# Kernel tuning notes

Hardware: AMD Instinct MI355X
Metric: run time of the kernel (lower is better)

## Reference

```python
import jax, jax.numpy as jnp
import numpy as np

N = 32768      # total nodes
E = 524288     # edges (avg degree 16)
HID = 256      # hidden_dim
H = 8          # heads
C = HID // H   # head dim = 32
G = 64         # graphs in batch
NPG = N // G   # nodes per graph = 512
EDIM = 2       # edge feature dim
NEG_SLOPE = 0.2  # PyG GATv2 default


def setup_inputs():
    key = jax.random.key(0)
    ks = jax.random.split(key, 12)
    s = 0.05
    return dict(
        x=jax.random.normal(ks[0], (N, HID), jnp.float32),
        edge_attr=jax.random.normal(ks[1], (E, EDIM), jnp.float32),
        # GATv2Conv params
        W_l=jax.random.normal(ks[2], (HID, HID), jnp.float32) * s,
        b_l=jnp.zeros((HID,), jnp.float32),
        W_r=jax.random.normal(ks[3], (HID, HID), jnp.float32) * s,
        b_r=jnp.zeros((HID,), jnp.float32),
        W_e=jax.random.normal(ks[4], (EDIM, HID), jnp.float32) * s,
        att=jax.random.normal(ks[5], (H, C), jnp.float32) * s,
        bias_gat=jnp.zeros((HID,), jnp.float32),
        # MultiheadAttention params (torch packed qkv layout)
        in_proj_w=jax.random.normal(ks[6], (3 * HID, HID), jnp.float32) * s,
        in_proj_b=jnp.zeros((3 * HID,), jnp.float32),
        out_proj_w=jax.random.normal(ks[7], (HID, HID), jnp.float32) * s,
        out_proj_b=jnp.zeros((HID,), jnp.float32),
        alpha_param=jnp.array(0.5, jnp.float32),
        # FFN
        W1=jax.random.normal(ks[8], (HID, 4 * HID), jnp.float32) * s,
        b1=jnp.zeros((4 * HID,), jnp.float32),
        W2=jax.random.normal(ks[9], (4 * HID, HID), jnp.float32) * s,
        b2=jnp.zeros((HID,), jnp.float32),
        # LayerNorms
        g1=jnp.ones((HID,), jnp.float32), be1=jnp.zeros((HID,), jnp.float32),
        g2=jnp.ones((HID,), jnp.float32), be2=jnp.zeros((HID,), jnp.float32),
        g3=jnp.ones((HID,), jnp.float32), be3=jnp.zeros((HID,), jnp.float32),
        edge_index=jax.random.randint(ks[10], (2, E), 0, N, jnp.int32),
        batch=jnp.repeat(jnp.arange(G, dtype=jnp.int32), NPG),
    )


def _ln(x, g, b, eps=1e-5):
    m = jnp.mean(x, -1, keepdims=True)
    v = jnp.mean((x - m) ** 2, -1, keepdims=True)
    return (x - m) * jax.lax.rsqrt(v + eps) * g + b


def _gatv2(x, edge_index, edge_attr, W_l, b_l, W_r, b_r, W_e, att, bias_gat):
    src, dst = edge_index[0], edge_index[1]
    # PyG add_self_loops with fill_value='mean': self-loop edge_attr at node i
    # is the mean of edge_attr over edges incoming to i (0 if none).
    deg = jax.ops.segment_sum(jnp.ones((E,), x.dtype), dst, num_segments=N)
    ea_mean = jax.ops.segment_sum(edge_attr, dst, num_segments=N) / jnp.maximum(deg, 1.0)[:, None]
    loop = jnp.arange(N, dtype=src.dtype)
    src2 = jnp.concatenate([src, loop])
    dst2 = jnp.concatenate([dst, loop])
    ea2 = jnp.concatenate([edge_attr, ea_mean], axis=0)  # [E+N, 2]
    xl = (x @ W_l + b_l).reshape(N, H, C)  # source transform (messages)
    xr = (x @ W_r + b_r).reshape(N, H, C)  # target transform
    ee = (ea2 @ W_e).reshape(-1, H, C)
    e = jax.nn.leaky_relu(xl[src2] + xr[dst2] + ee, NEG_SLOPE)  # [E+N, H, C]
    score = jnp.einsum('ehc,hc->eh', e, att)  # [E+N, H]
    # scatter softmax over incoming edges of each target node
    smax = jax.lax.stop_gradient(jax.ops.segment_max(score, dst2, num_segments=N))
    ex = jnp.exp(score - smax[dst2])
    ssum = jax.ops.segment_sum(ex, dst2, num_segments=N)
    alpha = ex / ssum[dst2]  # [E+N, H]
    out = jax.ops.segment_sum(alpha[:, :, None] * xl[src2], dst2, num_segments=N)
    return out.reshape(N, HID) + bias_gat


def _mha(xg, in_proj_w, in_proj_b, out_proj_w, out_proj_b):
    # xg: [G, NPG, HID]; torch nn.MultiheadAttention (batch_first, eval mode)
    qkv = xg @ in_proj_w.T + in_proj_b
    q, k, v = jnp.split(qkv, 3, axis=-1)
    q = q.reshape(G, NPG, H, C)
    k = k.reshape(G, NPG, H, C)
    v = v.reshape(G, NPG, H, C)
    scores = jnp.einsum('gqhd,gkhd->ghqk', q, k) / jnp.sqrt(jnp.float32(C))
    p = jax.nn.softmax(scores, axis=-1)
    o = jnp.einsum('ghqk,gkhd->gqhd', p, v).reshape(G, NPG, HID)
    return o @ out_proj_w.T + out_proj_b


def reference(x, edge_attr, W_l, b_l, W_r, b_r, W_e, att, bias_gat,
              in_proj_w, in_proj_b, out_proj_w, out_proj_b, alpha_param,
              W1, b1, W2, b2, g1, be1, g2, be2, g3, be3, edge_index, batch):
    local_out = _ln(
        _gatv2(x, edge_index, edge_attr, W_l, b_l, W_r, b_r, W_e, att, bias_gat),
        g1, be1)
    # batch is sorted with equal-sized graphs -> the per-graph ragged
    # attention loop equals one batched [G, NPG, NPG] attention
    xg = x.reshape(G, NPG, HID)
    global_out = _mha(xg, in_proj_w, in_proj_b, out_proj_w, out_proj_b).reshape(N, HID)
    global_out = _ln(global_out, g2, be2)
    a = jax.nn.sigmoid(alpha_param)
    combined = a * local_out + (1.0 - a) * global_out
    ffn = jax.nn.gelu(combined @ W1 + b1, approximate=False) @ W2 + b2
    return _ln(combined + ffn, g3, be3)
```

## Files before the change

kernel.cpp:

```cpp
#include <hip/hip_runtime.h>
#include <math.h>

#define N_NODES 32768
#define E_EDGES 524288
#define HIDDEN  256
#define NPG     512
#define NGRAPH  64
#define NHEAD   8
#define CDIM    32

typedef unsigned short bf16;
typedef __attribute__((ext_vector_type(8))) short short8;
typedef __attribute__((ext_vector_type(4))) float f4;

#define AS1 __attribute__((address_space(1)))
#define AS3 __attribute__((address_space(3)))

__device__ __forceinline__ void cp16(const bf16* g, bf16* l) {
    __builtin_amdgcn_global_load_lds((AS1 const unsigned int*)(const void*)g,
                                     (AS3 unsigned int*)(void*)l, 16, 0, 0);
}

__device__ inline float bf2f(unsigned short u) {
    union { unsigned int i; float f; } v; v.i = ((unsigned int)u) << 16; return v.f;
}
__device__ inline unsigned short f2bf(float f) {
    union { float f; unsigned int i; } v; v.f = f;
    unsigned int x = v.i;
    return (unsigned short)((x + 0x7FFFu + ((x >> 16) & 1u)) >> 16);
}
__device__ inline unsigned short f2bf_trunc(float f) {
    return (unsigned short)(__float_as_uint(f) >> 16);
}
__device__ inline float4 load4(const float* p) { return *(const float4*)p; }
__device__ inline float4 load4(const bf16* p) {
    ushort4 u = *(const ushort4*)p;
    return make_float4(bf2f(u.x), bf2f(u.y), bf2f(u.z), bf2f(u.w));
}
__device__ inline void store4(float* p, float4 v) { *(float4*)p = v; }
__device__ inline void store4(bf16* p, float4 v) {
    ushort4 u; u.x = f2bf(v.x); u.y = f2bf(v.y); u.z = f2bf(v.z); u.w = f2bf(v.w);
    *(ushort4*)p = u;
}


__global__ void zero_kernel(float* deg, float* ea_sum, int* fill) {
    int i = blockIdx.x * blockDim.x + threadIdx.x;
    if (i < 2 * N_NODES) ea_sum[i] = 0.0f;
    if (i < N_NODES) { deg[i] = 0.0f; fill[i] = 0; }
}

__global__ void deg_kernel(const int* __restrict__ ei, const float* __restrict__ edge_attr,
                           float* deg, float* ea_sum) {
    int e = blockIdx.x * blockDim.x + threadIdx.x;
    if (e >= E_EDGES) return;
    int d = ei[E_EDGES + e];
    atomicAdd(&deg[d], 1.0f);
    atomicAdd(&ea_sum[2 * d + 0], edge_attr[2 * e + 0]);
    atomicAdd(&ea_sum[2 * d + 1], edge_attr[2 * e + 1]);
}

__global__ __launch_bounds__(1024) void scan_kernel(const float* __restrict__ deg, int* row_ptr) {
    __shared__ int part[1024];
    int t = threadIdx.x;
    int base = t * 32;
    int loc[32];
    int s = 0;
    #pragma unroll
    for (int j = 0; j < 32; j++) {
        loc[j] = s;
        s += (int)deg[base + j] + 1;
    }
    int mysum = s;
    part[t] = s;
    __syncthreads();
    for (int off = 1; off < 1024; off <<= 1) {
        int v = 0;
        if (t >= off) v = part[t - off];
        __syncthreads();
        part[t] += v;
        __syncthreads();
    }
    int offset = part[t] - mysum;
    #pragma unroll
    for (int j = 0; j < 32; j++) row_ptr[base + j] = offset + loc[j];
    if (t == 1023) row_ptr[N_NODES] = part[1023];
}

__global__ void fill_kernel(const int* __restrict__ ei, const float* __restrict__ edge_attr,
                            const float* __restrict__ ea_sum, const float* __restrict__ deg,
                            const int* __restrict__ row_ptr, int* fill, int4* __restrict__ erec) {
    int tid = blockIdx.x * blockDim.x + threadIdx.x;
    if (tid >= E_EDGES + N_NODES) return;
    int d, src; float a0, a1;
    if (tid < E_EDGES) {
        d = ei[E_EDGES + tid];
        src = ei[tid];
        a0 = edge_attr[2 * tid + 0];
        a1 = edge_attr[2 * tid + 1];
    } else {
        d = tid - E_EDGES;
        src = d;
        float dm = fmaxf(deg[d], 1.0f);
        a0 = ea_sum[2 * d + 0] / dm;
        a1 = ea_sum[2 * d + 1] / dm;
    }
    int pos = row_ptr[d] + atomicAdd(&fill[d], 1);
    int4 r;
    r.x = src;
    r.y = __float_as_int(a0);
    r.z = __float_as_int(a1);
    r.w = 0;
    erec[pos] = r;
}

#define QSCALE 0.25506882685716462f
__global__ void convall(const float* __restrict__ x,
                        const float* __restrict__ W_l, const float* __restrict__ W_r,
                        const float* __restrict__ W1, const float* __restrict__ W2,
                        const float* __restrict__ in_proj_w, const float* __restrict__ out_proj_w,
                        const float* __restrict__ b_l, const float* __restrict__ b_r,
                        const float* __restrict__ in_proj_b,
                        bf16* xb, bf16* wcat, bf16* w1b, bf16* w2b,
                        bf16* wopb, float* bcat)
{
    int b = blockIdx.x, t = threadIdx.x;
    if (b < 8192) {
        int i = b * 256 + t;
        store4(&xb[i * 4], *(const float4*)&x[i * 4]);
    } else if (b < 8960) {
        int i = (b - 8192) * 256 + t;
        float v = in_proj_w[i];
        if (i < 65536) v *= QSCALE;
        wcat[i] = f2bf(v);
    } else if (b < 9216) {
        int i = (b - 8960) * 256 + t; int k = i >> 8, n = i & 255;
        wcat[(768 + n) * 256 + k] = f2bf(W_l[i]);
    } else if (b < 9472) {
        int i = (b - 9216) * 256 + t; int k = i >> 8, n = i & 255;
        wcat[(1024 + n) * 256 + k] = f2bf(W_r[i]);
    } else if (b < 10496) {
        int i = (b - 9472) * 256 + t; int k = i >> 10, n = i & 1023;
        w1b[n * 256 + k] = f2bf(W1[i]);
    } else if (b < 11520) {
        int i = (b - 10496) * 256 + t; int k = i >> 8, n = i & 255;
        w2b[n * 1024 + k] = f2bf(W2[i]);
    } else if (b < 11584) {
        int i = (b - 11520) * 256 + t;
        store4(&wopb[i * 4], *(const float4*)&out_proj_w[i * 4]);
    } else {
        #pragma unroll
        for (int j = 0; j < 5; j++) {
            int idx = j * 256 + t;
            float v;
            if (idx < 768) { v = in_proj_b[idx]; if (idx < 256) v *= QSCALE; }
            else if (idx < 1024) v = b_l[idx - 768];
            else v = b_r[idx - 1024];
            bcat[idx] = v;
        }
    }
}

template <int EPI>
__global__ __launch_bounds__(256) void mfma_gemm(
    const bf16* __restrict__ A, const bf16* __restrict__ Wb,
    const float* __restrict__ bias, const bf16* __restrict__ res,
    bf16* __restrict__ C, int M, int N, int K, bf16* __restrict__ d2)
{
    __shared__ bf16 lds[2 * 128 * 64];
    bf16* As = lds;
    bf16* Bs = lds + 128 * 64;
    int tid = threadIdx.x;
    int wave = tid >> 6, lane = tid & 63;
    int quad = lane >> 4, l16 = lane & 15;
    int n0 = blockIdx.x * 128, m0 = blockIdx.y * 128;
    int wm = (wave & 1) * 64, wn = (wave >> 1) * 64;

    f4 acc[4][4] = {};
    int srow = tid >> 3;
    int scol = (tid & 7) * 8;

    for (int k0 = 0; k0 < K; k0 += 64) {
        #pragma unroll
        for (int i = 0; i < 4; i++) {
            int row = i * 32 + srow;
            cp16(&A[(size_t)(m0 + row) * K + k0 + scol], &As[row * 64 + scol]);
            cp16(&Wb[(size_t)(n0 + row) * K + k0 + scol], &Bs[row * 64 + scol]);
        }
        __syncthreads();
        #pragma unroll
        for (int ks = 0; ks < 2; ks++) {
            short8 af[4], bfr[4];
            #pragma unroll
            for (int mt = 0; mt < 4; mt++)
                af[mt] = *(const short8*)&As[(wm + mt * 16 + l16) * 64 + ks * 32 + quad * 8];
            #pragma unroll
            for (int nt = 0; nt < 4; nt++)
                bfr[nt] = *(const short8*)&Bs[(wn + nt * 16 + l16) * 64 + ks * 32 + quad * 8];
            #pragma unroll
            for (int mt = 0; mt < 4; mt++)
                #pragma unroll
                for (int nt = 0; nt < 4; nt++)
                    acc[mt][nt] = __builtin_amdgcn_mfma_f32_16x16x32_bf16(
                        af[mt], bfr[nt], acc[mt][nt], 0, 0, 0);
        }
        __syncthreads();
    }

    float* epi = (float*)lds + wave * 16 * 68;
    int row = lane >> 2;
    int cb = (lane & 3) * 16;
    int gn = n0 + wn + cb;
    float bb[16];
    *(float4*)&bb[0]  = *(const float4*)&bias[gn + 0];
    *(float4*)&bb[4]  = *(const float4*)&bias[gn + 4];
    *(float4*)&bb[8]  = *(const float4*)&bias[gn + 8];
    *(float4*)&bb[12] = *(const float4*)&bias[gn + 12];

    for (int mt = 0; mt < 4; mt++) {
        #pragma unroll
        for (int nt = 0; nt < 4; nt++)
            #pragma unroll
            for (int r = 0; r < 4; r++)
                epi[(quad * 4 + r) * 68 + nt * 16 + l16] = acc[mt][nt][r];
        float vv[16];
        *(float4*)&vv[0]  = *(float4*)&epi[row * 68 + cb + 0];
        *(float4*)&vv[4]  = *(float4*)&epi[row * 68 + cb + 4];
        *(float4*)&vv[8]  = *(float4*)&epi[row * 68 + cb + 8];
        *(float4*)&vv[12] = *(float4*)&epi[row * 68 + cb + 12];
        int gm = m0 + wm + mt * 16 + row;
        #pragma unroll
        for (int j = 0; j < 16; j++) vv[j] += bb[j];
        if (EPI == 1) {
            #pragma unroll
            for (int j = 0; j < 16; j++)
                vv[j] = 0.5f * vv[j] * (1.0f + erff(vv[j] * 0.70710678118654752f));
        } else if (EPI == 4) {
            ushort rr[16];
            const bf16* rp = &res[(size_t)gm * N + gn];
            *(int4*)&rr[0] = *(const int4*)&rp[0];
            *(int4*)&rr[8] = *(const int4*)&rp[8];
            #pragma unroll
            for (int j = 0; j < 16; j++) vv[j] += bf2f(rr[j]);
            float* cf = (float*)C + (size_t)gm * N + gn;
            *(float4*)&cf[0]  = *(float4*)&vv[0];
            *(float4*)&cf[4]  = *(float4*)&vv[4];
            *(float4*)&cf[8]  = *(float4*)&vv[8];
            *(float4*)&cf[12] = *(float4*)&vv[12];
            continue;
        }
        ushort o16[16];
        #pragma unroll
        for (int j = 0; j < 16; j++) o16[j] = f2bf(vv[j]);
        bf16* cp;
        if (EPI == 5) {
            if (gn < 768) {
                cp = &C[(size_t)gm * 768 + gn];
            } else if (gn < 1024) {
                cp = &((bf16*)res)[(size_t)gm * 256 + (gn - 768)];
            } else {
                cp = &d2[(size_t)gm * 256 + (gn - 1024)];
            }
        } else {
            cp = &C[(size_t)gm * N + gn];
        }
        *(int4*)&cp[0] = *(int4*)&o16[0];
        *(int4*)&cp[8] = *(int4*)&o16[8];
    }
}

__global__ __launch_bounds__(256) void attn_mfma(
    const bf16* __restrict__ qkv, bf16* __restrict__ attnout)
{
    __shared__ bf16 Ks[128 * 40];
    __shared__ bf16 Vt[32 * 136];
    __shared__ bf16 Pb[4 * 64 * 40];

    int b = blockIdx.x;
    int g = b >> 4, h = (b >> 1) & 7, hlf = b & 1;
    int tid = threadIdx.x;
    int wave = tid >> 6, lane = tid & 63;
    int quad = lane >> 4, l16 = lane & 15;
    int qbase = hlf * 256 + wave * 64;
    bf16* Pw = &Pb[wave * 64 * 40];

    short8 qf[4];
    #pragma unroll
    for (int mt = 0; mt < 4; mt++) {
        size_t node = (size_t)(g * NPG + qbase + mt * 16 + l16);
        qf[mt] = *(const short8*)&qkv[node * 768 + h * CDIM + quad * 8];
    }

    f4 oacc[4][2] = {};
    float lacc[4][4] = {};

    for (int c = 0; c < 4; c++) {
        int kk0 = c * 128;
        __syncthreads();
        #pragma unroll
        for (int i = 0; i < 2; i++) {
            int idx = i * 256 + tid;
            int key = idx >> 2, kc = (idx & 3) * 8;
            *(int4*)&Ks[key * 40 + kc] =
                *(const int4*)&qkv[(size_t)(g * NPG + kk0 + key) * 768 + 256 + h * CDIM + kc];
        }
        {
            int key = tid >> 1, dblk = (tid & 1) * 16;
            ushort tmp[16];
            const bf16* vp = &qkv[(size_t)(g * NPG + kk0 + key) * 768 + 512 + h * CDIM + dblk];
            *(int4*)&tmp[0] = *(const int4*)&vp[0];
            *(int4*)&tmp[8] = *(const int4*)&vp[8];
            #pragma unroll
            for (int j = 0; j < 16; j++) Vt[(dblk + j) * 136 + key] = tmp[j];
        }
        __syncthreads();

        for (int sub = 0; sub < 4; sub++) {
            int ks0 = sub * 32;
            short8 kf[2];
            #pragma unroll
            for (int nt = 0; nt < 2; nt++)
                kf[nt] = *(const short8*)&Ks[(ks0 + nt * 16 + l16) * 40 + quad * 8];
            #pragma unroll
            for (int mt = 0; mt < 4; mt++) {
                #pragma unroll
                for (int nt = 0; nt < 2; nt++) {
                    f4 z = {0.f, 0.f, 0.f, 0.f};
                    f4 s = __builtin_amdgcn_mfma_f32_16x16x32_bf16(qf[mt], kf[nt], z, 0, 0, 0);
                    #pragma unroll
                    for (int r = 0; r < 4; r++) {
                        float p = exp2f(s[r]);
                        lacc[mt][r] += p;
                        Pw[(mt * 16 + quad * 4 + r) * 40 + nt * 16 + l16] = f2bf_trunc(p);
                    }
                }
            }
            short8 vf[2];
            #pragma unroll
            for (int dt = 0; dt < 2; dt++)
                vf[dt] = *(const short8*)&Vt[(dt * 16 + l16) * 136 + ks0 + quad * 8];
            #pragma unroll
            for (int mt = 0; mt < 4; mt++) {
                short8 pf = *(const short8*)&Pw[(mt * 16 + l16) * 40 + quad * 8];
                #pragma unroll
                for (int dt = 0; dt < 2; dt++)
                    oacc[mt][dt] = __builtin_amdgcn_mfma_f32_16x16x32_bf16(
                        pf, vf[dt], oacc[mt][dt], 0, 0, 0);
            }
        }
    }

    #pragma unroll
    for (int mt = 0; mt < 4; mt++)
        #pragma unroll
        for (int r = 0; r < 4; r++) {
            float l = lacc[mt][r];
            l += __shfl_xor(l, 1);
            l += __shfl_xor(l, 2);
            l += __shfl_xor(l, 4);
            l += __shfl_xor(l, 8);
            lacc[mt][r] = l;
        }

    #pragma unroll
    for (int mt = 0; mt < 4; mt++) {
        #pragma unroll
        for (int dt = 0; dt < 2; dt++) {
            #pragma unroll
            for (int r = 0; r < 4; r++) {
                float v = oacc[mt][dt][r] / lacc[mt][r];
                size_t node = (size_t)(g * NPG + qbase + mt * 16 + quad * 4 + r);
                attnout[node * HIDDEN + h * CDIM + dt * 16 + l16] = f2bf(v);
            }
        }
    }
}

__device__ __forceinline__ void fetchrec(
    int i, int re, int node, const int4* __restrict__ erec,
    int& s, float& a0, float& a1)
{
    if (i < re) {
        int4 r = erec[i];
        s = r.x; a0 = __int_as_float(r.y); a1 = __int_as_float(r.z);
    } else {
        s = node; a0 = 0.f; a1 = 0.f;
    }
}

__global__ __launch_bounds__(256) void gat_kernel(
    const bf16* __restrict__ xl, const bf16* __restrict__ xr,
    const int* __restrict__ row_ptr, const int4* __restrict__ erec,
    const float* __restrict__ W_e, const float* __restrict__ att,
    const float* __restrict__ bias_gat,
    const float* __restrict__ g1, const float* __restrict__ be1,
    bf16* __restrict__ out)
{
    __shared__ float pacc[2][260];
    __shared__ float plsum[2][64];
    int wave = threadIdx.x >> 6;
    int lane = threadIdx.x & 63;
    int nloc = wave >> 1, half = wave & 1;
    int node = blockIdx.x * 2 + nloc;
    int cb = lane * 4;

    float4 xr4 = load4(&xr[(size_t)node * 256 + cb]);
    float4 we0 = *(const float4*)&W_e[cb];
    float4 we1 = *(const float4*)&W_e[HIDDEN + cb];
    float4 at4 = *(const float4*)&att[cb];

    int rs = row_ptr[node], re = row_ptr[node + 1];

    float lsum = 0.f;
    float acc0 = 0.f, acc1 = 0.f, acc2 = 0.f, acc3 = 0.f;

    int i0 = rs + half;
    int s0, s1; float a00, a01, a10, a11;
    fetchrec(i0,     re, node, erec, s0, a00, a01);
    fetchrec(i0 + 2, re, node, erec, s1, a10, a11);
    ushort4 xu0 = *(const ushort4*)&xl[(size_t)s0 * 256 + cb];

    for (int i = i0; i < re; i += 2) {
        int s2; float a20, a21;
        fetchrec(i + 4, re, node, erec, s2, a20, a21);
        ushort4 xu1 = *(const ushort4*)&xl[(size_t)s1 * 256 + cb];

        float4 xl4 = make_float4(bf2f(xu0.x), bf2f(xu0.y), bf2f(xu0.z), bf2f(xu0.w));
        float t, p = 0.f;
        t = xl4.x + xr4.x + a00 * we0.x + a01 * we1.x; t = (t > 0.f) ? t : 0.2f * t; p += t * at4.x;
        t = xl4.y + xr4.y + a00 * we0.y + a01 * we1.y; t = (t > 0.f) ? t : 0.2f * t; p += t * at4.y;
        t = xl4.z + xr4.z + a00 * we0.z + a01 * we1.z; t = (t > 0.f) ? t : 0.2f * t; p += t * at4.z;
        t = xl4.w + xr4.w + a00 * we0.w + a01 * we1.w; t = (t > 0.f) ? t : 0.2f * t; p += t * at4.w;
        p += __shfl_xor(p, 1);
        p += __shfl_xor(p, 2);
        p += __shfl_xor(p, 4);
        float w = __expf(p);
        lsum += w;
        acc0 += w * xl4.x; acc1 += w * xl4.y; acc2 += w * xl4.z; acc3 += w * xl4.w;

        s0 = s1; a00 = a10; a01 = a11; xu0 = xu1;
        s1 = s2; a10 = a20; a11 = a21;
    }

    if (half) {
        plsum[nloc][lane] = lsum;
        pacc[nloc][cb + 0] = acc0; pacc[nloc][cb + 1] = acc1;
        pacc[nloc][cb + 2] = acc2; pacc[nloc][cb + 3] = acc3;
    }
    __syncthreads();
    if (!half) {
        lsum += plsum[nloc][lane];
        acc0 += pacc[nloc][cb + 0]; acc1 += pacc[nloc][cb + 1];
        acc2 += pacc[nloc][cb + 2]; acc3 += pacc[nloc][cb + 3];

        float inv = 1.0f / lsum;
        float v0 = acc0 * inv + bias_gat[cb + 0];
        float v1 = acc1 * inv + bias_gat[cb + 1];
        float v2 = acc2 * inv + bias_gat[cb + 2];
        float v3 = acc3 * inv + bias_gat[cb + 3];

        float s = v0 + v1 + v2 + v3;
        #pragma unroll
        for (int m = 1; m < 64; m <<= 1) s += __shfl_xor(s, m);
        float mean = s * (1.0f / 256.0f);
        float d0 = v0 - mean, d1 = v1 - mean, d2 = v2 - mean, d3 = v3 - mean;
        float sq = d0 * d0 + d1 * d1 + d2 * d2 + d3 * d3;
        #pragma unroll
        for (int m = 1; m < 64; m <<= 1) sq += __shfl_xor(sq, m);
        float rstd = rsqrtf(sq * (1.0f / 256.0f) + 1e-5f);
        float4 o;
        o.x = d0 * rstd * g1[cb + 0] + be1[cb + 0];
        o.y = d1 * rstd * g1[cb + 1] + be1[cb + 1];
        o.z = d2 * rstd * g1[cb + 2] + be1[cb + 2];
        o.w = d3 * rstd * g1[cb + 3] + be1[cb + 3];
        store4(&out[(size_t)node * HIDDEN + cb], o);
    }
}

__global__ __launch_bounds__(256) void combine_kernel(
    const bf16* __restrict__ gout, const bf16* __restrict__ localout,
    const float* __restrict__ alpha_p,
    const float* __restrict__ g2, const float* __restrict__ be2,
    bf16* __restrict__ combined)
{
    int wave = threadIdx.x >> 6;
    int lane = threadIdx.x & 63;
    int node = blockIdx.x * 4 + wave;
    int cb = lane * 4;
    float4 gv = load4(&gout[(size_t)node * HIDDEN + cb]);
    float s = gv.x + gv.y + gv.z + gv.w;
    #pragma unroll
    for (int m = 1; m < 64; m <<= 1) s += __shfl_xor(s, m);
    float mean = s * (1.0f / 256.0f);
    float d0 = gv.x - mean, d1 = gv.y - mean, d2 = gv.z - mean, d3 = gv.w - mean;
    float sq = d0 * d0 + d1 * d1 + d2 * d2 + d3 * d3;
    #pragma unroll
    for (int m = 1; m < 64; m <<= 1) sq += __shfl_xor(sq, m);
    float rstd = rsqrtf(sq * (1.0f / 256.0f) + 1e-5f);
    float n0 = d0 * rstd * g2[cb + 0] + be2[cb + 0];
    float n1 = d1 * rstd * g2[cb + 1] + be2[cb + 1];
    float n2 = d2 * rstd * g2[cb + 2] + be2[cb + 2];
    float n3 = d3 * rstd * g2[cb + 3] + be2[cb + 3];
    float a = 1.0f / (1.0f + __expf(-alpha_p[0]));
    float4 lv = load4(&localout[(size_t)node * HIDDEN + cb]);
    float4 o;
    o.x = a * lv.x + (1.0f - a) * n0;
    o.y = a * lv.y + (1.0f - a) * n1;
    o.z = a * lv.z + (1.0f - a) * n2;
    o.w = a * lv.w + (1.0f - a) * n3;
    store4(&combined[(size_t)node * HIDDEN + cb], o);
}

__global__ __launch_bounds__(256) void finalln_kernel(
    float* __restrict__ out,
    const float* __restrict__ g3, const float* __restrict__ be3)
{
    int wave = threadIdx.x >> 6;
    int lane = threadIdx.x & 63;
    int node = blockIdx.x * 4 + wave;
    int cb = lane * 4;
    float4 v = *(const float4*)&out[(size_t)node * HIDDEN + cb];
    float s = v.x + v.y + v.z + v.w;
    #pragma unroll
    for (int m = 1; m < 64; m <<= 1) s += __shfl_xor(s, m);
    float mean = s * (1.0f / 256.0f);
    float d0 = v.x - mean, d1 = v.y - mean, d2 = v.z - mean, d3 = v.w - mean;
    float sq = d0 * d0 + d1 * d1 + d2 * d2 + d3 * d3;
    #pragma unroll
    for (int m = 1; m < 64; m <<= 1) sq += __shfl_xor(sq, m);
    float rstd = rsqrtf(sq * (1.0f / 256.0f) + 1e-5f);
    float4 o;
    o.x = d0 * rstd * g3[cb + 0] + be3[cb + 0];
    o.y = d1 * rstd * g3[cb + 1] + be3[cb + 1];
    o.z = d2 * rstd * g3[cb + 2] + be3[cb + 2];
    o.w = d3 * rstd * g3[cb + 3] + be3[cb + 3];
    *(float4*)&out[(size_t)node * HIDDEN + cb] = o;
}

extern "C" void kernel_launch(void* const* d_in, const int* in_sizes, int n_in,
                              void* d_out, int out_size, void* d_ws, size_t ws_size,
                              hipStream_t stream) {
    const float* x          = (const float*)d_in[0];
    const float* edge_attr  = (const float*)d_in[1];
    const float* W_l        = (const float*)d_in[2];
    const float* b_l        = (const float*)d_in[3];
    const float* W_r        = (const float*)d_in[4];
    const float* b_r        = (const float*)d_in[5];
    const float* W_e        = (const float*)d_in[6];
    const float* att        = (const float*)d_in[7];
    const float* bias_gat   = (const float*)d_in[8];
    const float* in_proj_w  = (const float*)d_in[9];
    const float* in_proj_b  = (const float*)d_in[10];
    const float* out_proj_w = (const float*)d_in[11];
    const float* out_proj_b = (const float*)d_in[12];
    const float* alpha_p    = (const float*)d_in[13];
    const float* W1         = (const float*)d_in[14];
    const float* b1         = (const float*)d_in[15];
    const float* W2         = (const float*)d_in[16];
    const float* b2         = (const float*)d_in[17];
    const float* g1  = (const float*)d_in[18];
    const float* be1 = (const float*)d_in[19];
    const float* g2  = (const float*)d_in[20];
    const float* be2 = (const float*)d_in[21];
    const float* g3  = (const float*)d_in[22];
    const float* be3 = (const float*)d_in[23];
    const int* edge_index = (const int*)d_in[24];

    char* base = (char*)d_ws;
    const size_t MB = 1024 * 1024;
    const size_t KB = 1024;
    float* deg     = (float*)(base + 0);
    float* ea_sum  = (float*)(base + 131072);
    int*   fill    = (int*)  (base + 393216);
    int*   row_ptr = (int*)  (base + 524288);
    bf16* wcat = (bf16*)(base + 3 * MB);
    bf16* w1b  = (bf16*)(base + 3 * MB + 704 * KB);
    bf16* w2b  = (bf16*)(base + 3 * MB + 1216 * KB);
    bf16* wopb = (bf16*)(base + 3 * MB + 1728 * KB);
    float* bcat = (float*)(base + 5 * MB);
    bf16* xb       = (bf16*)(base + 8 * MB);
    bf16* qkv      = (bf16*)(base + 24 * MB);
    bf16* xl       = (bf16*)(base + 40 * MB);
    bf16* attnout  = (bf16*)(base + 8 * MB);
    bf16* gout     = (bf16*)(base + 24 * MB);
    bf16* localout = (bf16*)(base + 40 * MB);
    bf16* combined = (bf16*)(base + 56 * MB);
    bf16* h1       = (bf16*)(base + 120 * MB);
    int4* erec     = (int4*)(base + 88 * MB);
    bf16* xl_      = (bf16*)(base + 72 * MB);
    bf16* xr_      = (bf16*)(base + 104 * MB);
    float* out = (float*)d_out;

    zero_kernel<<<(2 * N_NODES + 255) / 256, 256, 0, stream>>>(deg, ea_sum, fill);
    deg_kernel<<<E_EDGES / 256, 256, 0, stream>>>(edge_index, edge_attr, deg, ea_sum);
    scan_kernel<<<1, 1024, 0, stream>>>(deg, row_ptr);
    fill_kernel<<<(E_EDGES + N_NODES + 255) / 256, 256, 0, stream>>>(
        edge_index, edge_attr, ea_sum, deg, row_ptr, fill, erec);

    convall<<<11585, 256, 0, stream>>>(x, W_l, W_r, W1, W2, in_proj_w, out_proj_w,
                                       b_l, b_r, in_proj_b,
                                       xb, wcat, w1b, w2b, wopb, bcat);

    mfma_gemm<5><<<dim3(10, 256), 256, 0, stream>>>(
        xb, wcat, bcat, xl_, qkv, N_NODES, 1280, 256, xr_);

    attn_mfma<<<NGRAPH * NHEAD * 2, 256, 0, stream>>>(qkv, attnout);
    gat_kernel<<<N_NODES / 2, 256, 0, stream>>>(
        xl_, xr_, row_ptr, erec, W_e, att, bias_gat, g1, be1, localout);

    mfma_gemm<0><<<dim3(2, 256), 256, 0, stream>>>(
        attnout, wopb, out_proj_b, (const bf16*)nullptr, gout, N_NODES, 256, 256, (bf16*)nullptr);

    combine_kernel<<<N_NODES / 4, 256, 0, stream>>>(
        gout, localout, alpha_p, g2, be2, combined);

    mfma_gemm<1><<<dim3(8, 256), 256, 0, stream>>>(
        combined, w1b, b1, (const bf16*)nullptr, h1, N_NODES, 1024, 256, (bf16*)nullptr);
    mfma_gemm<4><<<dim3(2, 256), 256, 0, stream>>>(
        h1, w2b, b2, combined, (bf16*)out, N_NODES, 256, 1024, (bf16*)nullptr);

    finalln_kernel<<<N_NODES / 4, 256, 0, stream>>>(out, g3, be3);
}
```

Before: 586.5 us.

## Fuse FFN up-projection, GELU, down-projection, residual and final LayerNorm into one kernel

Replaces the two FFN GEMM launches and the final LayerNorm kernel with a single kernel. Each block keeps a 64-row tile of the combined activations in swizzled LDS and streams W1 and W2 chunks through it, holding the 1024-wide hidden activation only in LDS. This removes the global round-trip of the h1 tensor and the fp32 output re-read. It also adds an XCD-aware block-index remap to the remaining GEMMs and replaces erff with a polynomial GELU approximation, trading some accuracy and lower occupancy (about 113KB LDS per block) for less memory traffic.

New measurement: 565.0 us. 1.04x faster.

```diff
diff --git a/kernel.cpp b/kernel.cpp
--- a/kernel.cpp
+++ b/kernel.cpp
@@ -41,6 +41,16 @@
 __device__ inline void store4(bf16* p, float4 v) {
     ushort4 u; u.x = f2bf(v.x); u.y = f2bf(v.y); u.z = f2bf(v.z); u.w = f2bf(v.w);
     *(ushort4*)p = u;
+}
+
+__device__ __forceinline__ float gelu_fast(float x) {
+    float z = fabsf(x) * 0.70710678118654752f;
+    float t = 1.0f / (1.0f + 0.3275911f * z);
+    float poly = t * (0.254829592f + t * (-0.284496736f + t * (1.421413741f
+               + t * (-1.453152027f + t * 1.061405429f))));
+    float erfv = 1.0f - poly * __expf(-z * z);
+    erfv = copysignf(erfv, x);
+    return 0.5f * x * (1.0f + erfv);
 }
 
 
@@ -173,7 +183,13 @@
     int tid = threadIdx.x;
     int wave = tid >> 6, lane = tid & 63;
     int quad = lane >> 4, l16 = lane & 15;
-    int n0 = blockIdx.x * 128, m0 = blockIdx.y * 128;
+    int nbx = gridDim.x;
+    int lid = blockIdx.y * nbx + blockIdx.x;
+    int chunk = (nbx * gridDim.y) >> 3;
+    int nlid = (lid & 7) * chunk + (lid >> 3);
+    int bx = nlid % nbx;
+    int by = nlid / nbx;
+    int n0 = bx * 128, m0 = by * 128;
     int wm = (wave & 1) * 64, wn = (wave >> 1) * 64;
 
     f4 acc[4][4] = {};
@@ -234,7 +250,7 @@
         if (EPI == 1) {
             #pragma unroll
             for (int j = 0; j < 16; j++)
-                vv[j] = 0.5f * vv[j] * (1.0f + erff(vv[j] * 0.70710678118654752f));
+                vv[j] = gelu_fast(vv[j]);
         } else if (EPI == 4) {
             ushort rr[16];
             const bf16* rp = &res[(size_t)gm * N + gn];
@@ -266,6 +282,163 @@
         }
         *(int4*)&cp[0] = *(int4*)&o16[0];
         *(int4*)&cp[8] = *(int4*)&o16[8];
+    }
+}
+
+__global__ __launch_bounds__(256) void ffn_fused(
+    const bf16* __restrict__ combined,
+    const bf16* __restrict__ w1b, const bf16* __restrict__ w2b,
+    const float* __restrict__ b1, const float* __restrict__ b2,
+    const float* __restrict__ g3, const float* __restrict__ be3,
+    float* __restrict__ out)
+{
+    __shared__ bf16 Asl[64 * 256];
+    __shared__ bf16 WB[128 * 256];
+    __shared__ bf16 H1[64 * 136];
+
+    char* Asl_c = (char*)Asl;
+    char* WB_c  = (char*)WB;
+    int tid = threadIdx.x;
+    int wave = tid >> 6, lane = tid & 63;
+    int quad = lane >> 4, l16 = lane & 15;
+    int m0 = blockIdx.x * 64;
+    int wn1 = wave * 32;
+    int wn2 = wave * 64;
+
+    #pragma unroll
+    for (int rr = 0; rr < 8; rr++) {
+        int o = rr * 4096 + tid * 16;
+        int L = o ^ (((o >> 9) & 7) << 4);
+        int row = L >> 9, colb = L & 511;
+        cp16((const bf16*)((const char*)combined + (size_t)(m0 + row) * 512 + colb),
+             (bf16*)(Asl_c + o));
+    }
+
+    f4 oacc[4][4] = {};
+
+    for (int j = 0; j < 8; j++) {
+        if (j) __syncthreads();
+        #pragma unroll
+        for (int rr = 0; rr < 16; rr++) {
+            int o = rr * 4096 + tid * 16;
+            int L = o ^ (((o >> 9) & 7) << 4);
+            int row = L >> 9, colb = L & 511;
+            cp16((const bf16*)((const char*)w1b + (size_t)(j * 128 + row) * 512 + colb),
+                 (bf16*)(WB_c + o));
+        }
+        __syncthreads();
+
+        f4 acc1[4][2] = {};
+        #pragma unroll
+        for (int ks = 0; ks < 8; ks++) {
+            short8 af[4], bf1[2];
+            #pragma unroll
+            for (int mt = 0; mt < 4; mt++) {
+                int r_ = mt * 16 + l16;
+                af[mt] = *(const short8*)(Asl_c +
+                    ((r_ * 512 + ks * 64 + quad * 16) ^ ((r_ & 7) << 4)));
+            }
+            #pragma unroll
+            for (int nt = 0; nt < 2; nt++) {
+                int r_ = wn1 + nt * 16 + l16;
+                bf1[nt] = *(const short8*)(WB_c +
+                    ((r_ * 512 + ks * 64 + quad * 16) ^ ((r_ & 7) << 4)));
+            }
+            #pragma unroll
+            for (int mt = 0; mt < 4; mt++)
+                #pragma unroll
+                for (int nt = 0; nt < 2; nt++)
+                    acc1[mt][nt] = __builtin_amdgcn_mfma_f32_16x16x32_bf16(
+                        af[mt], bf1[nt], acc1[mt][nt], 0, 0, 0);
+        }
+        float b1v0 = b1[j * 128 + wn1 + l16];
+        float b1v1 = b1[j * 128 + wn1 + 16 + l16];
+        __syncthreads();
+        #pragma unroll
+        for (int mt = 0; mt < 4; mt++)
+            #pragma unroll
+            for (int nt = 0; nt < 2; nt++) {
+                float bv = nt ? b1v1 : b1v0;
+                #pragma unroll
+                for (int r = 0; r < 4; r++) {
+                    float v = gelu_fast(acc1[mt][nt][r] + bv);
+                    H1[(mt * 16 + quad * 4 + r) * 136 + wn1 + nt * 16 + l16] = f2bf(v);
+                }
+            }
+        #pragma unroll
+        for (int rr = 0; rr < 16; rr++) {
+            int o = rr * 4096 + tid * 16;
+            int L = o ^ (((o >> 8) & 7) << 4);
+            int row = L >> 8, colb = L & 255;
+            cp16((const bf16*)((const char*)w2b + (size_t)row * 2048 + j * 256 + colb),
+                 (bf16*)(WB_c + o));
+        }
+        __syncthreads();
+        #pragma unroll
+        for (int ks = 0; ks < 4; ks++) {
+            short8 af2[4], bf2[4];
+            #pragma unroll
+            for (int mt = 0; mt < 4; mt++)
+                af2[mt] = *(const short8*)((char*)H1 +
+                    (mt * 16 + l16) * 272 + ks * 64 + quad * 16);
+            #pragma unroll
+            for (int nt = 0; nt < 4; nt++) {
+                int r_ = wn2 + nt * 16 + l16;
+                bf2[nt] = *(const short8*)(WB_c +
+                    ((r_ * 256 + ks * 64 + quad * 16) ^ ((r_ & 7) << 4)));
+            }
+            #pragma unroll
+            for (int mt = 0; mt < 4; mt++)
+                #pragma unroll
+                for (int nt = 0; nt < 4; nt++)
+                    oacc[mt][nt] = __builtin_amdgcn_mfma_f32_16x16x32_bf16(
+                        af2[mt], bf2[nt], oacc[mt][nt], 0, 0, 0);
+        }
+    }
+
+    #pragma unroll
+    for (int nt = 0; nt < 4; nt++) {
+        float b2v = b2[wn2 + nt * 16 + l16];
+        #pragma unroll
+        for (int mt = 0; mt < 4; mt++)
+            #pragma unroll
+            for (int r = 0; r < 4; r++) {
+                int rl = mt * 16 + quad * 4 + r;
+                int gn = wn2 + nt * 16 + l16;
+                int o = (rl * 512 + gn * 2) ^ ((rl & 7) << 4);
+                oacc[mt][nt][r] += b2v + bf2f(*(const bf16*)(Asl_c + o));
+            }
+    }
+    __syncthreads();
+    float* pre = (float*)WB;
+    #pragma unroll
+    for (int mt = 0; mt < 4; mt++)
+        #pragma unroll
+        for (int nt = 0; nt < 4; nt++)
+            #pragma unroll
+            for (int r = 0; r < 4; r++)
+                pre[(mt * 16 + quad * 4 + r) * 256 + wn2 + nt * 16 + l16] = oacc[mt][nt][r];
+    __syncthreads();
+    float4 gv  = *(const float4*)&g3[lane * 4];
+    float4 bev = *(const float4*)&be3[lane * 4];
+    for (int rr = 0; rr < 16; rr++) {
+        int row = wave * 16 + rr;
+        float4 v = *(const float4*)&pre[row * 256 + lane * 4];
+        float s = v.x + v.y + v.z + v.w;
+        #pragma unroll
+        for (int m = 1; m < 64; m <<= 1) s += __shfl_xor(s, m);
+        float mean = s * (1.0f / 256.0f);
+        float d0 = v.x - mean, d1 = v.y - mean, d2 = v.z - mean, d3 = v.w - mean;
+        float sq = d0 * d0 + d1 * d1 + d2 * d2 + d3 * d3;
+        #pragma unroll
+        for (int m = 1; m < 64; m <<= 1) sq += __shfl_xor(sq, m);
+        float rstd = rsqrtf(sq * (1.0f / 256.0f) + 1e-5f);
+        float4 o;
+        o.x = d0 * rstd * gv.x + bev.x;
+        o.y = d1 * rstd * gv.y + bev.y;
+        o.z = d2 * rstd * gv.z + bev.z;
+        o.w = d3 * rstd * gv.w + bev.w;
+        *(float4*)&out[(size_t)(m0 + row) * 256 + lane * 4] = o;
     }
 }
 
@@ -509,32 +682,6 @@
     o.z = a * lv.z + (1.0f - a) * n2;
     o.w = a * lv.w + (1.0f - a) * n3;
     store4(&combined[(size_t)node * HIDDEN + cb], o);
-}
-
-__global__ __launch_bounds__(256) void finalln_kernel(
-    float* __restrict__ out,
-    const float* __restrict__ g3, const float* __restrict__ be3)
-{
-    int wave = threadIdx.x >> 6;
-    int lane = threadIdx.x & 63;
-    int node = blockIdx.x * 4 + wave;
-    int cb = lane * 4;
-    float4 v = *(const float4*)&out[(size_t)node * HIDDEN + cb];
-    float s = v.x + v.y + v.z + v.w;
-    #pragma unroll
-    for (int m = 1; m < 64; m <<= 1) s += __shfl_xor(s, m);
-    float mean = s * (1.0f / 256.0f);
-    float d0 = v.x - mean, d1 = v.y - mean, d2 = v.z - mean, d3 = v.w - mean;
-    float sq = d0 * d0 + d1 * d1 + d2 * d2 + d3 * d3;
-    #pragma unroll
-    for (int m = 1; m < 64; m <<= 1) sq += __shfl_xor(sq, m);
-    float rstd = rsqrtf(sq * (1.0f / 256.0f) + 1e-5f);
-    float4 o;
-    o.x = d0 * rstd * g3[cb + 0] + be3[cb + 0];
-    o.y = d1 * rstd * g3[cb + 1] + be3[cb + 1];
-    o.z = d2 * rstd * g3[cb + 2] + be3[cb + 2];
-    o.w = d3 * rstd * g3[cb + 3] + be3[cb + 3];
-    *(float4*)&out[(size_t)node * HIDDEN + cb] = o;
 }
 
 extern "C" void kernel_launch(void* const* d_in, const int* in_sizes, int n_in,
@@ -580,12 +727,10 @@
     float* bcat = (float*)(base + 5 * MB);
     bf16* xb       = (bf16*)(base + 8 * MB);
     bf16* qkv      = (bf16*)(base + 24 * MB);
-    bf16* xl       = (bf16*)(base + 40 * MB);
     bf16* attnout  = (bf16*)(base + 8 * MB);
     bf16* gout     = (bf16*)(base + 24 * MB);
     bf16* localout = (bf16*)(base + 40 * MB);
     bf16* combined = (bf16*)(base + 56 * MB);
-    bf16* h1       = (bf16*)(base + 120 * MB);
     int4* erec     = (int4*)(base + 88 * MB);
     bf16* xl_      = (bf16*)(base + 72 * MB);
     bf16* xr_      = (bf16*)(base + 104 * MB);
@@ -614,10 +759,6 @@
     combine_kernel<<<N_NODES / 4, 256, 0, stream>>>(
         gout, localout, alpha_p, g2, be2, combined);
 
-    mfma_gemm<1><<<dim3(8, 256), 256, 0, stream>>>(
-        combined, w1b, b1, (const bf16*)nullptr, h1, N_NODES, 1024, 256, (bf16*)nullptr);
-    mfma_gemm<4><<<dim3(2, 256), 256, 0, stream>>>(
-        h1, w2b, b2, combined, (bf16*)out, N_NODES, 256, 1024, (bf16*)nullptr);
-
-    finalln_kernel<<<N_NODES / 4, 256, 0, stream>>>(out, g3, be3);
-}
+    ffn_fused<<<N_NODES / 64, 256, 0, stream>>>(
+        combined, w1b, w2b, b1, b2, g3, be3, out);
+}
```
